# Kernel tuning notes

Hardware: AMD Instinct MI355X
Metric: run time of the kernel (lower is better)

The kernel has to match this reference:

```python
import jax, jax.numpy as jnp
import numpy as np

EMB_DIM = 1024
H = 16
HEAD_DIM = EMB_DIM // H
B = 2
S = 2048  # enc and dec seq len
LN_EPS = 1e-5


def setup_inputs() -> dict:
    key = jax.random.key(0)
    ks = jax.random.split(key, 8)
    scale_in = 1.0 / np.sqrt(EMB_DIM)
    scale_o = 1.0 / np.sqrt(H * HEAD_DIM)
    return {
        "enc_out": jax.random.normal(ks[0], (B, S, EMB_DIM), jnp.float32),
        "dec_out": jax.random.normal(ks[1], (B, S, EMB_DIM), jnp.float32),
        # stacked per-head projections, equivalent to h separate Linear(emb_dim, head_dim, bias=False)
        "Wq": jax.random.uniform(ks[2], (H, EMB_DIM, HEAD_DIM), jnp.float32, -scale_in, scale_in),
        "Wk": jax.random.uniform(ks[3], (H, EMB_DIM, HEAD_DIM), jnp.float32, -scale_in, scale_in),
        "Wv": jax.random.uniform(ks[4], (H, EMB_DIM, HEAD_DIM), jnp.float32, -scale_in, scale_in),
        "Wo": jax.random.uniform(ks[5], (H * HEAD_DIM, EMB_DIM), jnp.float32, -scale_o, scale_o),
        "gamma": jnp.ones((EMB_DIM,), jnp.float32),
        "beta": jnp.zeros((EMB_DIM,), jnp.float32),
    }


def reference(enc_out, dec_out, Wq, Wk, Wv, Wo, gamma, beta):
    d = Wq.shape[-1]
    # per-head projections, batched over heads (same math as the Python loop)
    q = jnp.einsum('bse,hed->bhsd', dec_out, Wq)   # queries from decoder
    k = jnp.einsum('bte,hed->bhtd', enc_out, Wk)   # keys from encoder
    v = jnp.einsum('bte,hed->bhtd', enc_out, Wv)   # values from encoder
    scores = jnp.einsum('bhsd,bhtd->bhst', q, k) / jnp.sqrt(jnp.asarray(d, q.dtype))
    att = jax.nn.softmax(scores, axis=-1)
    ctx = jnp.einsum('bhst,bhtd->bhsd', att, v)
    b, h, s, hd = ctx.shape
    ctx = ctx.transpose(0, 2, 1, 3).reshape(b, s, h * hd)  # concat heads along feature dim
    transformed = ctx @ Wo  # dropout is identity in eval mode
    x = dec_out + transformed
    mu = jnp.mean(x, axis=-1, keepdims=True)
    var = jnp.mean(jnp.square(x - mu), axis=-1, keepdims=True)
    return (x - mu) * jax.lax.rsqrt(var + LN_EPS) * gamma + beta
```

## Files before the change

### kernel.cpp

```cpp
#include <hip/hip_runtime.h>
#include <hip/hip_bf16.h>

#define EMB   1024
#define NH    16
#define HD    64
#define SEQ   2048
#define SA    72

typedef __attribute__((ext_vector_type(8))) short          bf16x8;
typedef __attribute__((ext_vector_type(8))) unsigned short us8;
typedef __attribute__((ext_vector_type(4))) float          f32x4;

__device__ __forceinline__ float u2f(unsigned short u) {
    return __uint_as_float(((unsigned)u) << 16);
}
__device__ __forceinline__ unsigned short f2u(float f) {
    __hip_bfloat16 b = __float2bfloat16(f);
    return *reinterpret_cast<unsigned short*>(&b);
}
__device__ __forceinline__ bool detect_bf16(const void* gamma) {
    return ((const unsigned short*)gamma)[0] == 0x3F80;
}
__device__ __forceinline__ f32x4 fzero() {
    f32x4 v; v.x = v.y = v.z = v.w = 0.f; return v;
}
__device__ __forceinline__ void ld16f(const void* p, size_t idx, bool isbf, float* o) {
    if (isbf) {
        const unsigned short* b = (const unsigned short*)p + idx;
        us8 v0 = *(const us8*)b, v1 = *(const us8*)(b + 8);
        #pragma unroll
        for (int i = 0; i < 8; ++i) { o[i] = u2f(v0[i]); o[8 + i] = u2f(v1[i]); }
    } else {
        const float* f = (const float*)p + idx;
        #pragma unroll
        for (int i = 0; i < 4; ++i) {
            float4 v = *(const float4*)(f + 4 * i);
            o[4*i] = v.x; o[4*i+1] = v.y; o[4*i+2] = v.z; o[4*i+3] = v.w;
        }
    }
}
__device__ __forceinline__ float ld1f(const void* p, size_t i, bool isbf) {
    return isbf ? u2f(((const unsigned short*)p)[i]) : ((const float*)p)[i];
}
__device__ __forceinline__ float4 ld4(const void* p, size_t idx, bool isbf) {
    if (isbf) {
        ushort4 t = *reinterpret_cast<const ushort4*>((const unsigned short*)p + idx);
        return make_float4(u2f(t.x), u2f(t.y), u2f(t.z), u2f(t.w));
    }
    return *reinterpret_cast<const float4*>((const float*)p + idx);
}
__device__ __forceinline__ us8 pk8(const float* s) {
    us8 v;
    #pragma unroll
    for (int i = 0; i < 8; ++i) v[i] = f2u(s[i]);
    return v;
}
__device__ __forceinline__ f32x4 mfma16(bf16x8 a, bf16x8 b, f32x4 c) {
    return __builtin_amdgcn_mfma_f32_16x16x32_bf16(a, b, c, 0, 0, 0);
}
__device__ __forceinline__ bf16x8 mk8(unsigned w0, unsigned w1, unsigned w2, unsigned w3) {
    union { unsigned u[4]; bf16x8 v; } x;
    x.u[0] = w0; x.u[1] = w1; x.u[2] = w2; x.u[3] = w3;
    return x.v;
}
__device__ __forceinline__ float fexp2(float x) {
    return __builtin_amdgcn_exp2f(x);
}
__device__ __forceinline__ unsigned cvtpk(float lo, float hi) {
    unsigned r;
    asm("v_cvt_pk_bf16_f32 %0, %1, %2" : "=v"(r) : "v"(lo), "v"(hi));
    return r;
}
__device__ __forceinline__ void gl_lds16(const unsigned short* g, unsigned short* l) {
    __builtin_amdgcn_global_load_lds(
        (const __attribute__((address_space(1))) void*)g,
        (__attribute__((address_space(3))) void*)l,
        16, 0, 0);
}

#define QSCALE 0.18033688f

__global__ __launch_bounds__(256) void prep_kernel(
    const void* __restrict__ dec, const void* __restrict__ enc,
    const void* __restrict__ Wq, const void* __restrict__ Wk,
    const void* __restrict__ Wv, const void* __restrict__ Wo,
    const void* __restrict__ gamma,
    unsigned short* __restrict__ xb,
    unsigned short* __restrict__ wt,
    unsigned short* __restrict__ wot)
{
    const bool isbf = detect_bf16(gamma);
    const int blk = blockIdx.x;
    __shared__ unsigned short T[64][SA];

    if (blk < 2048) {
        const size_t HALF = (size_t)4096 * 1024;
        size_t idx = ((size_t)blk * 256 + threadIdx.x) * 16;
        const void* src; size_t off;
        if (idx < HALF) { src = dec; off = idx; } else { src = enc; off = idx - HALF; }
        float buf[16];
        ld16f(src, off, isbf, buf);
        *(us8*)&xb[idx]     = pk8(buf);
        *(us8*)&xb[idx + 8] = pk8(buf + 8);
    } else if (blk < 2816) {
        const int local = blk - 2048;
        const int which = local >> 8, h = (local >> 4) & 15, e0 = (local & 15) * 64;
        const void* W = (which == 0) ? Wq : (which == 1 ? Wk : Wv);
        const int sr = threadIdx.x >> 2, sc = (threadIdx.x & 3) * 16;

        float buf[16];
        ld16f(W, ((size_t)h * EMB + e0 + sr) * HD + sc, isbf, buf);
        #pragma unroll
        for (int i = 0; i < 16; ++i) T[sc + i][sr] = f2u(buf[i]);
        __syncthreads();
        us8 v0 = *(const us8*)&T[sr][sc];
        us8 v1 = *(const us8*)&T[sr][sc + 8];
        size_t o = (((size_t)which * NH + h) * HD + sr) * EMB + e0 + sc;
        *(us8*)&wt[o] = v0;
        *(us8*)&wt[o + 8] = v1;
    } else {
        const int local = blk - 2816;
        const int n0 = (local & 15) * 64, k0 = (local >> 4) * 64;
        const int sr = threadIdx.x >> 2, sc = (threadIdx.x & 3) * 16;

        float buf[16];
        ld16f(Wo, (size_t)(k0 + sr) * EMB + n0 + sc, isbf, buf);
        #pragma unroll
        for (int i = 0; i < 16; ++i) T[sc + i][sr] = f2u(buf[i]);
        __syncthreads();
        us8 v0 = *(const us8*)&T[sr][sc];
        us8 v1 = *(const us8*)&T[sr][sc + 8];
        size_t o = (size_t)(n0 + sr) * EMB + k0 + sc;
        *(us8*)&wot[o] = v0;
        *(us8*)&wot[o + 8] = v1;
    }
}

__global__ __launch_bounds__(256) void qkv_kernel(
    const unsigned short* __restrict__ xb,
    const unsigned short* __restrict__ wt,
    unsigned short* __restrict__ qo, unsigned short* __restrict__ ko,
    unsigned short* __restrict__ vt)
{
    const int id = blockIdx.x;
    const int xcd = id & 7, sl = id >> 3;
    const int m_t = xcd * 4 + (sl & 3);
    const int n_t = sl >> 2;
    const int m0 = m_t * 128, n0g = n_t * 128;
    const int which = n0g >> 10;
    const int nloc = n0g & 1023;
    const unsigned short* X = xb + ((which == 0) ? (size_t)0 : (size_t)4096 * 1024);

    __shared__ unsigned short smem[17408];
    unsigned short* const ldsA = smem;
    unsigned short* const ldsB = smem + 8192;

    const int tid = threadIdx.x, wv = tid >> 6, lane = tid & 63;
    const int lq = lane >> 4, lm = lane & 15;
    const int mw = (wv & 1) * 64, nw = (wv >> 1) * 64;

    const unsigned short* Wb = wt + (size_t)(which * 1024 + nloc) * EMB;

    const int seg0 = wv * 4;
    const int srow = lane >> 3;
    const int su   = (lane & 7) ^ srow;
    const unsigned short* aP[4];
    const unsigned short* bP[4];
    #pragma unroll
    for (int q = 0; q < 4; ++q) {
        const int s = seg0 + q;
        aP[q] = X  + (size_t)(m0 + 8 * s + srow) * EMB + su * 8;
        bP[q] = Wb + (size_t)(8 * s + srow) * EMB + su * 8;
    }

    f32x4 acc[4][4];
    #pragma unroll
    for (int i = 0; i < 4; ++i)
        #pragma unroll
        for (int j = 0; j < 4; ++j) acc[i][j] = fzero();

    const int xa = lm & 7;

    for (int k0 = 0; k0 < EMB; k0 += 64) {
        #pragma unroll
        for (int q = 0; q < 4; ++q) {
            gl_lds16(aP[q] + k0, ldsA + (seg0 + q) * 512);
            gl_lds16(bP[q] + k0, ldsB + (seg0 + q) * 512);
        }
        asm volatile("s_waitcnt vmcnt(0)" ::: "memory");
        __syncthreads();

        #pragma unroll
        for (int st = 0; st < 2; ++st) {
            const int u = (st * 4 + lq) ^ xa;
            bf16x8 af[4], bq[4];
            #pragma unroll
            for (int i = 0; i < 4; ++i)
                af[i] = *(const bf16x8*)(ldsA + (mw + i * 16 + lm) * 64 + u * 8);
            #pragma unroll
            for (int j = 0; j < 4; ++j)
                bq[j] = *(const bf16x8*)(ldsB + (nw + j * 16 + lm) * 64 + u * 8);
            #pragma unroll
            for (int i = 0; i < 4; ++i)
                #pragma unroll
                for (int j = 0; j < 4; ++j)
                    acc[i][j] = mfma16(af[i], bq[j], acc[i][j]);
        }
        __syncthreads();
    }

    const int b = m0 >> 11, s0 = m0 & (SEQ - 1);
    const float osc = (which == 0) ? QSCALE : 1.0f;
    if (which != 2) {
        unsigned short* Y = which ? ko : qo;
        #pragma unroll
        for (int i = 0; i < 4; ++i)
            #pragma unroll
            for (int j = 0; j < 4; ++j)
                #pragma unroll
                for (int r = 0; r < 4; ++r) {
                    int m = mw + i * 16 + lq * 4 + r;
                    int n = nloc + nw + j * 16 + lm;
                    int h = n >> 6, d = n & 63;
                    Y[(((size_t)b * NH + h) * SEQ + s0 + m) * HD + d] = f2u(acc[i][j][r] * osc);
                }
    } else {
        __syncthreads();
        unsigned short* vbuf = smem;
        #pragma unroll
        for (int i = 0; i < 4; ++i)
            #pragma unroll
            for (int j = 0; j < 4; ++j) {
                ushort4 p;
                p.x = f2u(acc[i][j][0]); p.y = f2u(acc[i][j][1]);
                p.z = f2u(acc[i][j][2]); p.w = f2u(acc[i][j][3]);
                *(ushort4*)&vbuf[(size_t)(nw + j * 16 + lm) * 136 + mw + i * 16 + lq * 4] = p;
            }
        __syncthreads();
        const int dd = tid >> 1, cc = (tid & 1) * 64;
        const int n = nloc + dd, h = n >> 6, d = n & 63;
        size_t o = (((size_t)b * NH + h) * HD + d) * SEQ + s0 + cc;
        #pragma unroll
        for (int jj = 0; jj < 8; ++jj)
            *(us8*)&vt[o + 8 * jj] = *(const us8*)&vbuf[(size_t)dd * 136 + cc + 8 * jj];
    }
}

__global__ __launch_bounds__(128) void attn_kernel(
    const unsigned short* __restrict__ qg,
    const unsigned short* __restrict__ kg,
    const unsigned short* __restrict__ vtg,
    unsigned short* __restrict__ ctx)
{
    __shared__ unsigned short Ks[2][4096];
    __shared__ unsigned short Vt[2][4096];

    const int tid = threadIdx.x, wv = tid >> 6, lane = tid & 63;
    const int lq = lane >> 4, lm = lane & 15;
    const int bh = blockIdx.x, q0 = blockIdx.y * 64;
    const unsigned short* Kg = kg + (size_t)bh * SEQ * HD;
    const unsigned short* Vg = vtg + (size_t)bh * HD * SEQ;

    const int srow = lane >> 3;
    const int su   = (lane & 7) ^ srow;
    const unsigned short* kSp[4];
    const unsigned short* vSp[4];
    #pragma unroll
    for (int j = 0; j < 4; ++j) {
        const int seg = wv + 2 * j;
        kSp[j] = Kg + (size_t)(8 * seg + srow) * HD  + su * 8;
        vSp[j] = Vg + (size_t)(8 * seg + srow) * SEQ + su * 8;
    }

    bf16x8 qf[2][2];
    #pragma unroll
    for (int s = 0; s < 2; ++s)
        #pragma unroll
        for (int st = 0; st < 2; ++st)
            qf[s][st] = *(const bf16x8*)(qg + (size_t)bh * SEQ * HD
                          + (size_t)(q0 + wv * 32 + s * 16 + lm) * HD + st * 32 + lq * 8);

    bf16x8 onesf;
    #pragma unroll
    for (int i = 0; i < 8; ++i) onesf[i] = (short)0x3F80;

    const f32x4 z = fzero();
    f32x4 Of[2][4], lacc[2];
    #pragma unroll
    for (int s = 0; s < 2; ++s) {
        lacc[s] = fzero();
        #pragma unroll
        for (int t = 0; t < 4; ++t) Of[s][t] = fzero();
    }

    const int xa = lm & 7;
    const int u0 = lq ^ xa;
    const int u1 = (4 + lq) ^ xa;

    #pragma unroll
    for (int j = 0; j < 4; ++j) {
        gl_lds16(kSp[j], &Ks[0][(wv + 2 * j) * 512]);
        gl_lds16(vSp[j], &Vt[0][(wv + 2 * j) * 512]);
    }

    for (int it = 0; it < SEQ / 64; ++it) {
        const int cur = it & 1;
        asm volatile("s_waitcnt vmcnt(0)" ::: "memory");
        __syncthreads();
        if (it + 1 < SEQ / 64) {
            const size_t ko = (size_t)(it + 1) * 64 * HD;
            const int    vo = (it + 1) * 64;
            #pragma unroll
            for (int j = 0; j < 4; ++j) {
                gl_lds16(kSp[j] + ko, &Ks[cur ^ 1][(wv + 2 * j) * 512]);
                gl_lds16(vSp[j] + vo, &Vt[cur ^ 1][(wv + 2 * j) * 512]);
            }
        }

        f32x4 sf[2][4];
        #pragma unroll
        for (int tt = 0; tt < 4; ++tt) {
            bf16x8 kf = *(const bf16x8*)&Ks[cur][(lm + 16 * tt) * 64 + u0 * 8];
            sf[0][tt] = mfma16(kf, qf[0][0], z);
            sf[1][tt] = mfma16(kf, qf[1][0], z);
        }
        #pragma unroll
        for (int tt = 0; tt < 4; ++tt) {
            bf16x8 kf = *(const bf16x8*)&Ks[cur][(lm + 16 * tt) * 64 + u1 * 8];
            sf[0][tt] = mfma16(kf, qf[0][1], sf[0][tt]);
            sf[1][tt] = mfma16(kf, qf[1][1], sf[1][tt]);
        }

        unsigned pw[2][4][2];
        #pragma unroll
        for (int s = 0; s < 2; ++s)
            #pragma unroll
            for (int tt = 0; tt < 4; ++tt) {
                pw[s][tt][0] = cvtpk(fexp2(sf[s][tt][0]), fexp2(sf[s][tt][1]));
                pw[s][tt][1] = cvtpk(fexp2(sf[s][tt][2]), fexp2(sf[s][tt][3]));
            }
        #pragma unroll
        for (int s = 0; s < 2; ++s)
            #pragma unroll
            for (int a = 0; a < 2; ++a)
                #pragma unroll
                for (int c = 0; c < 2; ++c)
                    asm("v_permlane32_swap_b32 %0, %1"
                        : "+v"(pw[s][2 * a][c]), "+v"(pw[s][2 * a + 1][c]));
        #pragma unroll
        for (int s = 0; s < 2; ++s)
            #pragma unroll
            for (int a = 0; a < 2; ++a)
                #pragma unroll
                for (int c = 0; c < 2; ++c)
                    asm("v_permlane16_swap_b32 %0, %1"
                        : "+v"(pw[s][2 * a][c]), "+v"(pw[s][2 * a + 1][c]));

        #pragma unroll
        for (int st = 0; st < 2; ++st) {
            const int u = st ? u1 : u0;
            bf16x8 pf0 = mk8(pw[0][2 * st][0], pw[0][2 * st][1],
                             pw[0][2 * st + 1][0], pw[0][2 * st + 1][1]);
            bf16x8 pf1 = mk8(pw[1][2 * st][0], pw[1][2 * st][1],
                             pw[1][2 * st + 1][0], pw[1][2 * st + 1][1]);
            #pragma unroll
            for (int t = 0; t < 4; ++t) {
                bf16x8 vf = *(const bf16x8*)&Vt[cur][(lm + 16 * t) * 64 + u * 8];
                Of[0][t] = mfma16(pf0, vf, Of[0][t]);
                Of[1][t] = mfma16(pf1, vf, Of[1][t]);
            }
            lacc[0] = mfma16(pf0, onesf, lacc[0]);
            lacc[1] = mfma16(pf1, onesf, lacc[1]);
        }
    }

    const int b = bh >> 4, h = bh & 15;
    #pragma unroll
    for (int s = 0; s < 2; ++s)
        #pragma unroll
        for (int r = 0; r < 4; ++r) {
            float inv = 1.0f / lacc[s][r];
            int srow2 = q0 + wv * 32 + s * 16 + lq * 4 + r;
            #pragma unroll
            for (int t = 0; t < 4; ++t) {
                int d = lm + 16 * t;
                ctx[((size_t)b * SEQ + srow2) * EMB + h * HD + d] = f2u(Of[s][t][r] * inv);
            }
        }
}

__global__ __launch_bounds__(256) void oproj_kernel(
    const unsigned short* __restrict__ ctx,
    const unsigned short* __restrict__ wot,
    const void* __restrict__ dec, const void* __restrict__ gamma,
    float* __restrict__ x)
{
    const bool isbf = detect_bf16(gamma);
    const int id = blockIdx.x;
    const int xcd = id & 7, sl = id >> 3;
    const int m0 = (xcd * 4 + (sl & 3)) * 128;
    const int n0 = (sl >> 2) * 128;

    __shared__ unsigned short smem[16384];
    unsigned short* const ldsA = smem;
    unsigned short* const ldsB = smem + 8192;

    const int tid = threadIdx.x, wv = tid >> 6, lane = tid & 63;
    const int lq = lane >> 4, lm = lane & 15;
    const int mw = (wv & 1) * 64, nw = (wv >> 1) * 64;

    const int seg0 = wv * 4;
    const int srow = lane >> 3;
    const int su   = (lane & 7) ^ srow;
    const unsigned short* aP[4];
    const unsigned short* bP[4];
    #pragma unroll
    for (int q = 0; q < 4; ++q) {
        const int s = seg0 + q;
        aP[q] = ctx + (size_t)(m0 + 8 * s + srow) * EMB + su * 8;
        bP[q] = wot + (size_t)(n0 + 8 * s + srow) * EMB + su * 8;
    }

    f32x4 acc[4][4];
    #pragma unroll
    for (int i = 0; i < 4; ++i)
        #pragma unroll
        for (int j = 0; j < 4; ++j) acc[i][j] = fzero();

    const int xa = lm & 7;

    for (int k0 = 0; k0 < EMB; k0 += 64) {
        #pragma unroll
        for (int q = 0; q < 4; ++q) {
            gl_lds16(aP[q] + k0, ldsA + (seg0 + q) * 512);
            gl_lds16(bP[q] + k0, ldsB + (seg0 + q) * 512);
        }
        asm volatile("s_waitcnt vmcnt(0)" ::: "memory");
        __syncthreads();

        #pragma unroll
        for (int st = 0; st < 2; ++st) {
            const int u = (st * 4 + lq) ^ xa;
            bf16x8 af[4], bq[4];
            #pragma unroll
            for (int i = 0; i < 4; ++i)
                af[i] = *(const bf16x8*)(ldsA + (mw + i * 16 + lm) * 64 + u * 8);
            #pragma unroll
            for (int j = 0; j < 4; ++j)
                bq[j] = *(const bf16x8*)(ldsB + (nw + j * 16 + lm) * 64 + u * 8);
            #pragma unroll
            for (int i = 0; i < 4; ++i)
                #pragma unroll
                for (int j = 0; j < 4; ++j)
                    acc[i][j] = mfma16(af[i], bq[j], acc[i][j]);
        }
        __syncthreads();
    }

    #pragma unroll
    for (int i = 0; i < 4; ++i)
        #pragma unroll
        for (int j = 0; j < 4; ++j)
            #pragma unroll
            for (int r = 0; r < 4; ++r) {
                int m = m0 + mw + i * 16 + lq * 4 + r;
                int n = n0 + nw + j * 16 + lm;
                x[(size_t)m * EMB + n] = acc[i][j][r] + ld1f(dec, (size_t)m * EMB + n, isbf);
            }
}

__global__ __launch_bounds__(256) void ln_kernel(
    const float* __restrict__ x,
    const void* __restrict__ gamma,
    const void* __restrict__ beta,
    void* __restrict__ out)
{
    const bool isbf = detect_bf16(gamma);
    const int row = blockIdx.x;
    const int tid = threadIdx.x;
    const float* xr = x + (size_t)row * EMB;

    float4 xv = *reinterpret_cast<const float4*>(&xr[tid * 4]);
    float s1 = xv.x + xv.y + xv.z + xv.w;
    float s2 = xv.x * xv.x + xv.y * xv.y + xv.z * xv.z + xv.w * xv.w;

    #pragma unroll
    for (int off = 32; off > 0; off >>= 1) {
        s1 += __shfl_down(s1, off);
        s2 += __shfl_down(s2, off);
    }
    __shared__ float w1[4], w2[4];
    const int wid = tid >> 6, lane = tid & 63;
    if (lane == 0) { w1[wid] = s1; w2[wid] = s2; }
    __syncthreads();
    s1 = w1[0] + w1[1] + w1[2] + w1[3];
    s2 = w2[0] + w2[1] + w2[2] + w2[3];

    const float mu  = s1 * (1.0f / EMB);
    const float var = s2 * (1.0f / EMB) - mu * mu;
    const float rs  = rsqrtf(var + 1e-5f);

    float4 gv = ld4(gamma, (size_t)tid * 4, isbf);
    float4 bv = ld4(beta,  (size_t)tid * 4, isbf);
    float4 r;
    r.x = (xv.x - mu) * rs * gv.x + bv.x;
    r.y = (xv.y - mu) * rs * gv.y + bv.y;
    r.z = (xv.z - mu) * rs * gv.z + bv.z;
    r.w = (xv.w - mu) * rs * gv.w + bv.w;

    size_t o = (size_t)row * EMB + tid * 4;
    if (isbf) {
        ushort4 w;
        w.x = f2u(r.x); w.y = f2u(r.y); w.z = f2u(r.z); w.w = f2u(r.w);
        *reinterpret_cast<ushort4*>((unsigned short*)out + o) = w;
    } else {
        *reinterpret_cast<float4*>((float*)out + o) = r;
    }
}

extern "C" void kernel_launch(void* const* d_in, const int* in_sizes, int n_in,
                              void* d_out, int out_size, void* d_ws, size_t ws_size,
                              hipStream_t stream)
{
    const void* enc   = d_in[0];
    const void* dec   = d_in[1];
    const void* Wq    = d_in[2];
    const void* Wk    = d_in[3];
    const void* Wv    = d_in[4];
    const void* Wo    = d_in[5];
    const void* gamma = d_in[6];
    const void* beta  = d_in[7];

    char* w = (char*)d_ws;
    unsigned short* qws  = (unsigned short*)(w);
    unsigned short* kws  = (unsigned short*)(w + (size_t)8  * 1024 * 1024);
    unsigned short* vtws = (unsigned short*)(w + (size_t)16 * 1024 * 1024);
    unsigned short* wtws = (unsigned short*)(w + (size_t)24 * 1024 * 1024);
    unsigned short* wotw = (unsigned short*)(w + (size_t)30 * 1024 * 1024);
    float*          xws  = (float*)         (w);
    unsigned short* xbuf = (unsigned short*)d_out;
    unsigned short* cws  = (unsigned short*)d_out;

    prep_kernel  <<<3072,          256, 0, stream>>>(dec, enc, Wq, Wk, Wv, Wo,
                                                     gamma, xbuf, wtws, wotw);
    qkv_kernel   <<<768,           256, 0, stream>>>(xbuf, wtws, qws, kws, vtws);
    attn_kernel  <<<dim3(32, 32),  128, 0, stream>>>(qws, kws, vtws, cws);
    oproj_kernel <<<256,           256, 0, stream>>>(cws, wotw, dec, gamma, xws);
    ln_kernel    <<<4096,          256, 0, stream>>>(xws, gamma, beta, d_out);
}
```

Measured before the change: 249.9 us.

## Load attention K/V directly from global into registers with K prefetch ping-pong

The attention kernel no longer stages K and V^T tiles in double-buffered shared memory with async global-to-LDS copies and per-iteration barriers. Each wave now reads its K and V fragments straight from global memory into registers. K fragments for the next tile are prefetched into a register ping-pong pair while the current tile's scores are computed, and the loop is unrolled by two to alternate the buffers. This removes the LDS traffic, the vmcnt waits and the __syncthreads. In exchange, the two waves of a block each fetch the same K/V data from cache, V reads are less coalesced, register pressure rises, and the final prefetch reads one tile past the end of each head's K.

```diff
diff --git a/kernel.cpp b/kernel.cpp
--- a/kernel.cpp
+++ b/kernel.cpp
@@ -246,31 +246,99 @@
     }
 }
 
+__device__ __forceinline__ void attn_loadk(
+    const unsigned short* kB, int t0, bf16x8 (&kf)[2][4])
+{
+    #pragma unroll
+    for (int st = 0; st < 2; ++st)
+        #pragma unroll
+        for (int tt = 0; tt < 4; ++tt)
+            kf[st][tt] = *(const bf16x8*)(kB + (size_t)(t0 + 16 * tt) * HD + st * 32);
+}
+
+__device__ __forceinline__ void attn_iter(
+    int it, int itn,
+    const unsigned short* kB, const unsigned short* vB,
+    bf16x8 (&kfc)[2][4], bf16x8 (&kfn)[2][4],
+    const bf16x8 (&qf)[2][2], bf16x8 onesf,
+    f32x4 (&Of)[2][4], f32x4 (&lacc)[2])
+{
+    const int t0 = it * 64;
+    bf16x8 vf[2][4];
+    #pragma unroll
+    for (int st = 0; st < 2; ++st)
+        #pragma unroll
+        for (int t = 0; t < 4; ++t)
+            vf[st][t] = *(const bf16x8*)(vB + (size_t)(16 * t) * SEQ + t0 + st * 32);
+
+    const f32x4 z = fzero();
+    f32x4 sf[2][4];
+    #pragma unroll
+    for (int tt = 0; tt < 4; ++tt) {
+        sf[0][tt] = mfma16(kfc[0][tt], qf[0][0], z);
+        sf[1][tt] = mfma16(kfc[0][tt], qf[1][0], z);
+    }
+    #pragma unroll
+    for (int tt = 0; tt < 4; ++tt) {
+        sf[0][tt] = mfma16(kfc[1][tt], qf[0][1], sf[0][tt]);
+        sf[1][tt] = mfma16(kfc[1][tt], qf[1][1], sf[1][tt]);
+    }
+
+    attn_loadk(kB, itn * 64, kfn);
+
+    unsigned pw[2][4][2];
+    #pragma unroll
+    for (int s = 0; s < 2; ++s)
+        #pragma unroll
+        for (int tt = 0; tt < 4; ++tt) {
+            pw[s][tt][0] = cvtpk(fexp2(sf[s][tt][0]), fexp2(sf[s][tt][1]));
+            pw[s][tt][1] = cvtpk(fexp2(sf[s][tt][2]), fexp2(sf[s][tt][3]));
+        }
+    #pragma unroll
+    for (int s = 0; s < 2; ++s)
+        #pragma unroll
+        for (int a = 0; a < 2; ++a)
+            #pragma unroll
+            for (int c = 0; c < 2; ++c)
+                asm("v_permlane32_swap_b32 %0, %1"
+                    : "+v"(pw[s][2 * a][c]), "+v"(pw[s][2 * a + 1][c]));
+    #pragma unroll
+    for (int s = 0; s < 2; ++s)
+        #pragma unroll
+        for (int a = 0; a < 2; ++a)
+            #pragma unroll
+            for (int c = 0; c < 2; ++c)
+                asm("v_permlane16_swap_b32 %0, %1"
+                    : "+v"(pw[s][2 * a][c]), "+v"(pw[s][2 * a + 1][c]));
+
+    #pragma unroll
+    for (int st = 0; st < 2; ++st) {
+        bf16x8 pf0 = mk8(pw[0][2 * st][0], pw[0][2 * st][1],
+                         pw[0][2 * st + 1][0], pw[0][2 * st + 1][1]);
+        bf16x8 pf1 = mk8(pw[1][2 * st][0], pw[1][2 * st][1],
+                         pw[1][2 * st + 1][0], pw[1][2 * st + 1][1]);
+        #pragma unroll
+        for (int t = 0; t < 4; ++t) {
+            Of[0][t] = mfma16(pf0, vf[st][t], Of[0][t]);
+            Of[1][t] = mfma16(pf1, vf[st][t], Of[1][t]);
+        }
+        lacc[0] = mfma16(pf0, onesf, lacc[0]);
+        lacc[1] = mfma16(pf1, onesf, lacc[1]);
+    }
+}
+
 __global__ __launch_bounds__(128) void attn_kernel(
     const unsigned short* __restrict__ qg,
     const unsigned short* __restrict__ kg,
     const unsigned short* __restrict__ vtg,
     unsigned short* __restrict__ ctx)
 {
-    __shared__ unsigned short Ks[2][4096];
-    __shared__ unsigned short Vt[2][4096];
-
     const int tid = threadIdx.x, wv = tid >> 6, lane = tid & 63;
     const int lq = lane >> 4, lm = lane & 15;
     const int bh = blockIdx.x, q0 = blockIdx.y * 64;
-    const unsigned short* Kg = kg + (size_t)bh * SEQ * HD;
-    const unsigned short* Vg = vtg + (size_t)bh * HD * SEQ;
-
-    const int srow = lane >> 3;
-    const int su   = (lane & 7) ^ srow;
-    const unsigned short* kSp[4];
-    const unsigned short* vSp[4];
-    #pragma unroll
-    for (int j = 0; j < 4; ++j) {
-        const int seg = wv + 2 * j;
-        kSp[j] = Kg + (size_t)(8 * seg + srow) * HD  + su * 8;
-        vSp[j] = Vg + (size_t)(8 * seg + srow) * SEQ + su * 8;
-    }
+
+    const unsigned short* kB = kg + (size_t)bh * SEQ * HD + (size_t)lm * HD + lq * 8;
+    const unsigned short* vB = vtg + (size_t)bh * HD * SEQ + (size_t)lm * SEQ + lq * 8;
 
     bf16x8 qf[2][2];
     #pragma unroll
@@ -284,7 +352,6 @@
     #pragma unroll
     for (int i = 0; i < 8; ++i) onesf[i] = (short)0x3F80;
 
-    const f32x4 z = fzero();
     f32x4 Of[2][4], lacc[2];
     #pragma unroll
     for (int s = 0; s < 2; ++s) {
@@ -293,85 +360,11 @@
         for (int t = 0; t < 4; ++t) Of[s][t] = fzero();
     }
 
-    const int xa = lm & 7;
-    const int u0 = lq ^ xa;
-    const int u1 = (4 + lq) ^ xa;
-
-    #pragma unroll
-    for (int j = 0; j < 4; ++j) {
-        gl_lds16(kSp[j], &Ks[0][(wv + 2 * j) * 512]);
-        gl_lds16(vSp[j], &Vt[0][(wv + 2 * j) * 512]);
-    }
-
-    for (int it = 0; it < SEQ / 64; ++it) {
-        const int cur = it & 1;
-        asm volatile("s_waitcnt vmcnt(0)" ::: "memory");
-        __syncthreads();
-        if (it + 1 < SEQ / 64) {
-            const size_t ko = (size_t)(it + 1) * 64 * HD;
-            const int    vo = (it + 1) * 64;
-            #pragma unroll
-            for (int j = 0; j < 4; ++j) {
-                gl_lds16(kSp[j] + ko, &Ks[cur ^ 1][(wv + 2 * j) * 512]);
-                gl_lds16(vSp[j] + vo, &Vt[cur ^ 1][(wv + 2 * j) * 512]);
-            }
-        }
-
-        f32x4 sf[2][4];
-        #pragma unroll
-        for (int tt = 0; tt < 4; ++tt) {
-            bf16x8 kf = *(const bf16x8*)&Ks[cur][(lm + 16 * tt) * 64 + u0 * 8];
-            sf[0][tt] = mfma16(kf, qf[0][0], z);
-            sf[1][tt] = mfma16(kf, qf[1][0], z);
-        }
-        #pragma unroll
-        for (int tt = 0; tt < 4; ++tt) {
-            bf16x8 kf = *(const bf16x8*)&Ks[cur][(lm + 16 * tt) * 64 + u1 * 8];
-            sf[0][tt] = mfma16(kf, qf[0][1], sf[0][tt]);
-            sf[1][tt] = mfma16(kf, qf[1][1], sf[1][tt]);
-        }
-
-        unsigned pw[2][4][2];
-        #pragma unroll
-        for (int s = 0; s < 2; ++s)
-            #pragma unroll
-            for (int tt = 0; tt < 4; ++tt) {
-                pw[s][tt][0] = cvtpk(fexp2(sf[s][tt][0]), fexp2(sf[s][tt][1]));
-                pw[s][tt][1] = cvtpk(fexp2(sf[s][tt][2]), fexp2(sf[s][tt][3]));
-            }
-        #pragma unroll
-        for (int s = 0; s < 2; ++s)
-            #pragma unroll
-            for (int a = 0; a < 2; ++a)
-                #pragma unroll
-                for (int c = 0; c < 2; ++c)
-                    asm("v_permlane32_swap_b32 %0, %1"
-                        : "+v"(pw[s][2 * a][c]), "+v"(pw[s][2 * a + 1][c]));
-        #pragma unroll
-        for (int s = 0; s < 2; ++s)
-            #pragma unroll
-            for (int a = 0; a < 2; ++a)
-                #pragma unroll
-                for (int c = 0; c < 2; ++c)
-                    asm("v_permlane16_swap_b32 %0, %1"
-                        : "+v"(pw[s][2 * a][c]), "+v"(pw[s][2 * a + 1][c]));
-
-        #pragma unroll
-        for (int st = 0; st < 2; ++st) {
-            const int u = st ? u1 : u0;
-            bf16x8 pf0 = mk8(pw[0][2 * st][0], pw[0][2 * st][1],
-                             pw[0][2 * st + 1][0], pw[0][2 * st + 1][1]);
-            bf16x8 pf1 = mk8(pw[1][2 * st][0], pw[1][2 * st][1],
-                             pw[1][2 * st + 1][0], pw[1][2 * st + 1][1]);
-            #pragma unroll
-            for (int t = 0; t < 4; ++t) {
-                bf16x8 vf = *(const bf16x8*)&Vt[cur][(lm + 16 * t) * 64 + u * 8];
-                Of[0][t] = mfma16(pf0, vf, Of[0][t]);
-                Of[1][t] = mfma16(pf1, vf, Of[1][t]);
-            }
-            lacc[0] = mfma16(pf0, onesf, lacc[0]);
-            lacc[1] = mfma16(pf1, onesf, lacc[1]);
-        }
+    bf16x8 kfa[2][4], kfb[2][4];
+    attn_loadk(kB, 0, kfa);
+    for (int it = 0; it < SEQ / 64; it += 2) {
+        attn_iter(it,     it + 1, kB, vB, kfa, kfb, qf, onesf, Of, lacc);
+        attn_iter(it + 1, it + 2, kB, vB, kfb, kfa, qf, onesf, Of, lacc);
     }
 
     const int b = bh >> 4, h = bh & 15;
```

Result: slower. 303.4 us (+21.4%).
